# Kernel optimization log

Hardware: AMD Instinct MI355X
Metric: run time of the kernel (lower is better)

The kernel has to match this reference:

```python
import jax, jax.numpy as jnp
import numpy as np


def setup_inputs() -> dict:
    key = jax.random.key(0)
    k1, k2 = jax.random.split(key)
    x = jax.random.normal(k1, (32, 128, 112, 112), dtype=jnp.float32)
    weight = jax.random.normal(k2, (256, 128, 3, 3), dtype=jnp.float32)
    return {"x": x, "weight": weight}


def reference(x, weight):
    # Equivalent to torch unfold + einsum: valid (no padding), stride-1
    # cross-correlation conv2d with no bias.
    # x: [B, Cin, H, W], weight: [Cout, Cin, kh, kw] -> [B, Cout, H-kh+1, W-kw+1]
    return jax.lax.conv_general_dilated(
        x, weight,
        window_strides=(1, 1),
        padding="VALID",
        dimension_numbers=("NCHW", "OIHW", "NCHW"),
    )
```

## Files before the change

kernel.cpp:

```cpp
#include <hip/hip_runtime.h>

typedef __attribute__((ext_vector_type(8))) short short8;
typedef __attribute__((ext_vector_type(4))) float f32x4;
typedef unsigned int u32;

#define CIN   128
#define COUT  256
#define H     112
#define W     112
#define OH    110
#define OW    110
#define KHW   9
#define TH    8
#define TW    32
#define IWW   34
#define NPIX  340
#define XB    (NPIX*8*16)
#define WB    16384
#define ROWB  (IWW*128)

__device__ __forceinline__ short f2b(float f) {
  unsigned u = __builtin_bit_cast(unsigned, f);
  unsigned r = (u + 0x7FFFu + ((u >> 16) & 1u)) >> 16;
  return (short)r;
}

__device__ __forceinline__ void gload16(const void* g, void* l) {
  __builtin_amdgcn_global_load_lds(
      (const __attribute__((address_space(1))) u32*)g,
      (__attribute__((address_space(3))) u32*)l, 16, 0, 0);
}


template<bool XT, bool WT>
__global__ __launch_bounds__(256, 2)
void conv_main(const float* __restrict__ x, const float* __restrict__ wgt,
               const short* __restrict__ wt, const short* __restrict__ xt,
               const short* __restrict__ zp, float* __restrict__ out) {
  __shared__ __align__(16) char smem[XB + 2*WB];
  char* sx = smem;
  char* sw = smem + XB;

  const int tid = threadIdx.x;

  const int nb  = gridDim.x;
  const int swz = (blockIdx.x & 7) * (nb >> 3) + (blockIdx.x >> 3);
  const int b    = swz / 112;
  const int rem  = swz - b * 112;
  const int cblk = rem / 56;
  const int rem2 = rem - cblk * 56;
  const int t_w  = rem2 / 14;
  const int t_h  = rem2 - t_w * 14;
  const int h0 = t_h * TH, w0 = t_w * TW;

  auto stage_x = [&](int hh) {
    if (XT) {
      const short* xtb = xt + (size_t)b * (H*W*CIN);
      #pragma unroll
      for (int it = 0; it < 11; ++it) {
        int u = it*256 + tid;
        if (u < 8*NPIX) {
          int p = u >> 3;
          int iy = p / IWW, ix = p - iy * IWW;
          int Geff = (u & 7) ^ (ix & 7);
          int gy = h0 + iy, gx = w0 + ix;
          const short* src = (gy < H && gx < W)
              ? xtb + ((size_t)gy*W + gx)*CIN + hh*64 + Geff*8
              : zp;
          gload16(src, sx + u*16);
        }
      }
    } else {
      const float* xh = x + (size_t)b * CIN * (H*W) + (size_t)(hh*64) * (H*W);
      for (int u = tid; u < 8 * NPIX; u += 256) {
        int G = u / NPIX, p = u - G * NPIX;
        int iy = p / IWW, ix = p - iy * IWW;
        int gy = h0 + iy, gx = w0 + ix;
        short8 v = {0,0,0,0,0,0,0,0};
        if (gy < H && gx < W) {
          const float* s = xh + (size_t)(G*8) * (H*W) + gy * W + gx;
          #pragma unroll
          for (int j = 0; j < 8; ++j) v[j] = f2b(s[j * (H*W)]);
        }
        *(short8*)(sx + p*128 + ((G ^ (ix & 7)) << 4)) = v;
      }
    }
  };

  auto stage_w = [&](int st, int buf) {
    int hh = st / 9, tap = st - hh * 9;
    if (WT) {
      const short* base = wt + (size_t)tap * (COUT*CIN)
                             + (size_t)(cblk*128) * CIN + hh * 64;
      #pragma unroll
      for (int it = 0; it < 4; ++it) {
        int slot = it * 256 + tid;
        int c = slot >> 3, gsw = (slot & 7) ^ (c & 7);
        gload16(base + c * CIN + gsw * 8, sw + buf*WB + slot * 16);
      }
    } else {
      #pragma unroll
      for (int it = 0; it < 4; ++it) {
        int slot = it * 256 + tid;
        int c = slot >> 3, gsw = (slot & 7) ^ (c & 7);
        int cout = cblk*128 + c;
        short8 v;
        #pragma unroll
        for (int j = 0; j < 8; ++j) {
          int cin = hh*64 + gsw*8 + j;
          v[j] = f2b(wgt[cout*(CIN*KHW) + cin*KHW + tap]);
        }
        *(short8*)(sw + buf*WB + slot * 16) = v;
      }
    }
  };

  const int lane = tid & 63;
  const int wid  = tid >> 6;
  const int wm = wid >> 1;
  const int wn = wid & 1;
  const int l15 = lane & 15;
  const int kgrp = lane >> 4;

  int arow[4];
  #pragma unroll
  for (int mi = 0; mi < 4; ++mi) arow[mi] = (wm*64 + mi*16 + l15) * 128;
  const int l7 = l15 & 7;

  f32x4 acc[4][8] = {};

  stage_x(0);
  stage_w(0, 0);
  __syncthreads();

  for (int st = 0; st < 18; ++st) {
    const int tap = st % 9;
    const int kh = tap / 3, kw = tap - (tap/3)*3;
    const char* swb = sw + (st & 1) * WB;
    const int brow = (4*wn + kh) * ROWB;

    #pragma unroll
    for (int s = 0; s < 2; ++s) {
      const int g = s*4 + kgrp;
      const int akey = (g ^ l7) << 4;
      const int bkey = (g ^ ((l15 + kw) & 7)) << 4;
      const char* ab = swb + akey;
      const char* bb0 = sx + brow + (l15 + kw)*128 + bkey;
      const char* bb1 = bb0 + 16*128;

      short8 a[4];
      #pragma unroll
      for (int mi = 0; mi < 4; ++mi)
        a[mi] = *(const short8*)(ab + arow[mi]);
      short8 bf[8];
      #pragma unroll
      for (int r = 0; r < 4; ++r) {
        bf[2*r]   = *(const short8*)(bb0 + r*ROWB);
        bf[2*r+1] = *(const short8*)(bb1 + r*ROWB);
      }

      if (s == 0 && st + 1 < 18)
        stage_w(st + 1, (st + 1) & 1);

      __builtin_amdgcn_s_setprio(1);
      #pragma unroll
      for (int mi = 0; mi < 4; ++mi)
        #pragma unroll
        for (int ni = 0; ni < 8; ++ni)
          acc[mi][ni] = __builtin_amdgcn_mfma_f32_16x16x32_bf16(a[mi], bf[ni], acc[mi][ni], 0, 0, 0);
      __builtin_amdgcn_s_setprio(0);
    }

    if (st == 8) {
      __syncthreads();
      stage_x(1);
      __syncthreads();
    } else {
      __syncthreads();
    }
  }

  float* ob = out + (size_t)b * COUT * (OH*OW);
  #pragma unroll
  for (int ni = 0; ni < 8; ++ni) {
    int oh = h0 + 4*wn + (ni >> 1);
    int ow = w0 + (ni & 1)*16 + l15;
    if (oh < OH && ow < OW) {
      #pragma unroll
      for (int mi = 0; mi < 4; ++mi) {
        #pragma unroll
        for (int r = 0; r < 4; ++r) {
          int cout = cblk*128 + wm*64 + mi*16 + kgrp*4 + r;
          ob[(size_t)cout*(OH*OW) + oh*OW + ow] = acc[mi][ni][r];
        }
      }
    }
  }
}

__global__ void wprep(const float* __restrict__ wgt, short* __restrict__ wt,
                      short* __restrict__ zp) {
  int idx = blockIdx.x * 256 + threadIdx.x;
  if (idx < 128) zp[idx] = 0;
  if (idx >= KHW*COUT*CIN) return;
  int khw  = idx / (COUT*CIN);
  int rem  = idx - khw*(COUT*CIN);
  int cout = rem >> 7, cin = rem & 127;
  wt[idx] = f2b(wgt[cout*(CIN*KHW) + cin*KHW + khw]);
}

__global__ __launch_bounds__(256)
void xprep(const float* __restrict__ x, short* __restrict__ xt) {
  __shared__ short lsh[CIN * 113];
  const int bh = blockIdx.x;
  const int b = bh / H, h = bh - b * H;
  const float* src = x + ((size_t)b * CIN * H + h) * W;
  for (int u = threadIdx.x; u < CIN * W; u += 256) {
    int c = u / W, w = u - c * W;
    lsh[c * 113 + w] = f2b(src[(size_t)c * (H*W) + w]);
  }
  __syncthreads();
  short* dst = xt + (size_t)bh * (W * CIN);
  for (int o = threadIdx.x; o < W * CIN / 8; o += 256) {
    int w = o >> 4, s = o & 15;
    short8 v;
    #pragma unroll
    for (int j = 0; j < 8; ++j) v[j] = lsh[(s*8 + j) * 113 + w];
    *(short8*)(dst + o * 8) = v;
  }
}

extern "C" void kernel_launch(void* const* d_in, const int* in_sizes, int n_in,
                              void* d_out, int out_size, void* d_ws, size_t ws_size,
                              hipStream_t stream) {
  const float* x   = (const float*)d_in[0];
  const float* wgt = (const float*)d_in[1];
  float* out = (float*)d_out;
  const size_t wt_bytes = (size_t)(KHW*COUT*CIN) * sizeof(short);
  const size_t zp_bytes = 256;
  const size_t xt_bytes = (size_t)32 * H * W * CIN * sizeof(short);
  dim3 grid(3584);
  if (ws_size >= wt_bytes + zp_bytes + xt_bytes) {
    short* wt = (short*)d_ws;
    short* zp = (short*)((char*)d_ws + wt_bytes);
    short* xt = (short*)((char*)d_ws + wt_bytes + zp_bytes);
    wprep<<<(KHW*COUT*CIN + 255)/256, 256, 0, stream>>>(wgt, wt, zp);
    xprep<<<32 * H, 256, 0, stream>>>(x, xt);
    conv_main<true, true><<<grid, 256, 0, stream>>>(x, wgt, wt, xt, zp, out);
  } else if (ws_size >= wt_bytes + zp_bytes) {
    short* wt = (short*)d_ws;
    short* zp = (short*)((char*)d_ws + wt_bytes);
    wprep<<<(KHW*COUT*CIN + 255)/256, 256, 0, stream>>>(wgt, wt, zp);
    conv_main<false, true><<<grid, 256, 0, stream>>>(x, wgt, wt, nullptr, zp, out);
  } else {
    conv_main<false, false><<<grid, 256, 0, stream>>>(x, wgt, nullptr, nullptr, nullptr, out);
  }
}
```

Baseline: 339.2 us.

## Load weight fragments directly from global memory in MFMA layout, drop LDS staging

```diff
diff --git a/kernel.cpp b/kernel.cpp
--- a/kernel.cpp
+++ b/kernel.cpp
@@ -16,7 +16,6 @@
 #define IWW   34
 #define NPIX  340
 #define XB    (NPIX*8*16)
-#define WB    16384
 #define ROWB  (IWW*128)
 
 __device__ __forceinline__ short f2b(float f) {
@@ -35,11 +34,9 @@
 template<bool XT, bool WT>
 __global__ __launch_bounds__(256, 2)
 void conv_main(const float* __restrict__ x, const float* __restrict__ wgt,
-               const short* __restrict__ wt, const short* __restrict__ xt,
+               const short* __restrict__ wt2, const short* __restrict__ xt,
                const short* __restrict__ zp, float* __restrict__ out) {
-  __shared__ __align__(16) char smem[XB + 2*WB];
-  char* sx = smem;
-  char* sw = smem + XB;
+  __shared__ __align__(16) char sx[XB];
 
   const int tid = threadIdx.x;
 
@@ -87,34 +84,6 @@
     }
   };
 
-  auto stage_w = [&](int st, int buf) {
-    int hh = st / 9, tap = st - hh * 9;
-    if (WT) {
-      const short* base = wt + (size_t)tap * (COUT*CIN)
-                             + (size_t)(cblk*128) * CIN + hh * 64;
-      #pragma unroll
-      for (int it = 0; it < 4; ++it) {
-        int slot = it * 256 + tid;
-        int c = slot >> 3, gsw = (slot & 7) ^ (c & 7);
-        gload16(base + c * CIN + gsw * 8, sw + buf*WB + slot * 16);
-      }
-    } else {
-      #pragma unroll
-      for (int it = 0; it < 4; ++it) {
-        int slot = it * 256 + tid;
-        int c = slot >> 3, gsw = (slot & 7) ^ (c & 7);
-        int cout = cblk*128 + c;
-        short8 v;
-        #pragma unroll
-        for (int j = 0; j < 8; ++j) {
-          int cin = hh*64 + gsw*8 + j;
-          v[j] = f2b(wgt[cout*(CIN*KHW) + cin*KHW + tap]);
-        }
-        *(short8*)(sw + buf*WB + slot * 16) = v;
-      }
-    }
-  };
-
   const int lane = tid & 63;
   const int wid  = tid >> 6;
   const int wm = wid >> 1;
@@ -122,61 +91,61 @@
   const int l15 = lane & 15;
   const int kgrp = lane >> 4;
 
-  int arow[4];
+  const int acout8 = (cblk*128 + wm*64 + l15) * 8;
+
+  f32x4 acc[4][8] = {};
+
+  stage_x(0);
+  __syncthreads();
+
   #pragma unroll
-  for (int mi = 0; mi < 4; ++mi) arow[mi] = (wm*64 + mi*16 + l15) * 128;
-  const int l7 = l15 & 7;
-
-  f32x4 acc[4][8] = {};
-
-  stage_x(0);
-  stage_w(0, 0);
-  __syncthreads();
-
-  for (int st = 0; st < 18; ++st) {
-    const int tap = st % 9;
-    const int kh = tap / 3, kw = tap - (tap/3)*3;
-    const char* swb = sw + (st & 1) * WB;
-    const int brow = (4*wn + kh) * ROWB;
-
-    #pragma unroll
-    for (int s = 0; s < 2; ++s) {
-      const int g = s*4 + kgrp;
-      const int akey = (g ^ l7) << 4;
-      const int bkey = (g ^ ((l15 + kw) & 7)) << 4;
-      const char* ab = swb + akey;
-      const char* bb0 = sx + brow + (l15 + kw)*128 + bkey;
-      const char* bb1 = bb0 + 16*128;
-
-      short8 a[4];
-      #pragma unroll
-      for (int mi = 0; mi < 4; ++mi)
-        a[mi] = *(const short8*)(ab + arow[mi]);
-      short8 bf[8];
-      #pragma unroll
-      for (int r = 0; r < 4; ++r) {
-        bf[2*r]   = *(const short8*)(bb0 + r*ROWB);
-        bf[2*r+1] = *(const short8*)(bb1 + r*ROWB);
-      }
-
-      if (s == 0 && st + 1 < 18)
-        stage_w(st + 1, (st + 1) & 1);
-
-      __builtin_amdgcn_s_setprio(1);
-      #pragma unroll
-      for (int mi = 0; mi < 4; ++mi)
-        #pragma unroll
-        for (int ni = 0; ni < 8; ++ni)
-          acc[mi][ni] = __builtin_amdgcn_mfma_f32_16x16x32_bf16(a[mi], bf[ni], acc[mi][ni], 0, 0, 0);
-      __builtin_amdgcn_s_setprio(0);
-    }
-
-    if (st == 8) {
+  for (int hh = 0; hh < 2; ++hh) {
+    if (hh == 1) {
       __syncthreads();
       stage_x(1);
       __syncthreads();
-    } else {
-      __syncthreads();
+    }
+    #pragma unroll
+    for (int tap = 0; tap < 9; ++tap) {
+      const int kh = tap / 3, kw = tap - (tap/3)*3;
+      #pragma unroll
+      for (int s = 0; s < 2; ++s) {
+        const int g = s*4 + kgrp;
+        short8 a[4];
+        if (WT) {
+          const short* ap = wt2 + ((size_t)(tap*16 + hh*8) + g) * 2048 + acout8;
+          #pragma unroll
+          for (int mi = 0; mi < 4; ++mi)
+            a[mi] = *(const short8*)(ap + mi*128);
+        } else {
+          #pragma unroll
+          for (int mi = 0; mi < 4; ++mi) {
+            int cout = cblk*128 + wm*64 + mi*16 + l15;
+            #pragma unroll
+            for (int j = 0; j < 8; ++j) {
+              int cin = hh*64 + g*8 + j;
+              a[mi][j] = f2b(wgt[cout*(CIN*KHW) + cin*KHW + tap]);
+            }
+          }
+        }
+        const int bkey = (g ^ ((l15 + kw) & 7)) << 4;
+        const char* bb0 = sx + (4*wn + kh)*ROWB + (l15 + kw)*128 + bkey;
+        const char* bb1 = bb0 + 16*128;
+        short8 bf[8];
+        #pragma unroll
+        for (int r = 0; r < 4; ++r) {
+          bf[2*r]   = *(const short8*)(bb0 + r*ROWB);
+          bf[2*r+1] = *(const short8*)(bb1 + r*ROWB);
+        }
+        __builtin_amdgcn_s_setprio(1);
+        #pragma unroll
+        for (int mi = 0; mi < 4; ++mi)
+          #pragma unroll
+          for (int ni = 0; ni < 8; ++ni)
+            acc[mi][ni] = __builtin_amdgcn_mfma_f32_16x16x32_bf16(
+                a[mi], bf[ni], acc[mi][ni], 0, 0, 0);
+        __builtin_amdgcn_s_setprio(0);
+      }
     }
   }
 
@@ -198,15 +167,19 @@
   }
 }
 
-__global__ void wprep(const float* __restrict__ wgt, short* __restrict__ wt,
+__global__ void wprep(const float* __restrict__ wgt, short* __restrict__ wt2,
                       short* __restrict__ zp) {
   int idx = blockIdx.x * 256 + threadIdx.x;
   if (idx < 128) zp[idx] = 0;
-  if (idx >= KHW*COUT*CIN) return;
-  int khw  = idx / (COUT*CIN);
-  int rem  = idx - khw*(COUT*CIN);
-  int cout = rem >> 7, cin = rem & 127;
-  wt[idx] = f2b(wgt[cout*(CIN*KHW) + cin*KHW + khw]);
+  if (idx >= KHW*16*COUT) return;
+  int tap  = idx / (16*COUT);
+  int rem  = idx - tap*(16*COUT);
+  int G    = rem >> 8, cout = rem & 255;
+  short8 v;
+  #pragma unroll
+  for (int j = 0; j < 8; ++j)
+    v[j] = f2b(wgt[cout*(CIN*KHW) + (G*8 + j)*KHW + tap]);
+  *(short8*)(wt2 + (size_t)idx * 8) = v;
 }
 
 __global__ __launch_bounds__(256)
@@ -241,17 +214,17 @@
   const size_t xt_bytes = (size_t)32 * H * W * CIN * sizeof(short);
   dim3 grid(3584);
   if (ws_size >= wt_bytes + zp_bytes + xt_bytes) {
-    short* wt = (short*)d_ws;
-    short* zp = (short*)((char*)d_ws + wt_bytes);
-    short* xt = (short*)((char*)d_ws + wt_bytes + zp_bytes);
-    wprep<<<(KHW*COUT*CIN + 255)/256, 256, 0, stream>>>(wgt, wt, zp);
+    short* wt2 = (short*)d_ws;
+    short* zp  = (short*)((char*)d_ws + wt_bytes);
+    short* xt  = (short*)((char*)d_ws + wt_bytes + zp_bytes);
+    wprep<<<(KHW*16*COUT + 255)/256, 256, 0, stream>>>(wgt, wt2, zp);
     xprep<<<32 * H, 256, 0, stream>>>(x, xt);
-    conv_main<true, true><<<grid, 256, 0, stream>>>(x, wgt, wt, xt, zp, out);
+    conv_main<true, true><<<grid, 256, 0, stream>>>(x, wgt, wt2, xt, zp, out);
   } else if (ws_size >= wt_bytes + zp_bytes) {
-    short* wt = (short*)d_ws;
-    short* zp = (short*)((char*)d_ws + wt_bytes);
-    wprep<<<(KHW*COUT*CIN + 255)/256, 256, 0, stream>>>(wgt, wt, zp);
-    conv_main<false, true><<<grid, 256, 0, stream>>>(x, wgt, wt, nullptr, zp, out);
+    short* wt2 = (short*)d_ws;
+    short* zp  = (short*)((char*)d_ws + wt_bytes);
+    wprep<<<(KHW*16*COUT + 255)/256, 256, 0, stream>>>(wgt, wt2, zp);
+    conv_main<false, true><<<grid, 256, 0, stream>>>(x, wgt, wt2, nullptr, zp, out);
   } else {
     conv_main<false, false><<<grid, 256, 0, stream>>>(x, wgt, nullptr, nullptr, nullptr, out);
   }
```

After: 369.9 us. 1.09x slower.
